# Optimization experiments

Hardware: AMD Instinct MI355X
Metric: run time of the kernel (lower is better)

Reference implementation:

```python
import jax, jax.numpy as jnp
import numpy as np

N_HEAD = 16

def setup_inputs() -> dict:
    key = jax.random.key(0)
    k1, k2, k3 = jax.random.split(key, 3)
    B, T, C = 4, 2048, 1024
    x = jax.random.normal(k1, (B, T, C), dtype=jnp.float32)
    w_attn = jax.random.normal(k2, (C, 3 * C), dtype=jnp.float32) * 0.02
    w_o = jax.random.normal(k3, (C, C), dtype=jnp.float32) * 0.02
    return {"x": x, "w_attn": w_attn, "w_o": w_o}

def reference(x, w_attn, w_o):
    B, T, C = x.shape
    H = N_HEAD
    hs = C // H
    qkv = x @ w_attn  # [B,T,3C]
    q, k, v = jnp.split(qkv, 3, axis=-1)
    # [B,H,T,hs]
    q = q.reshape(B, T, H, hs).transpose(0, 2, 1, 3)
    k = k.reshape(B, T, H, hs).transpose(0, 2, 1, 3)
    v = v.reshape(B, T, H, hs).transpose(0, 2, 1, 3)
    att = jnp.einsum('bhqd,bhkd->bhqk', q, k) * (1.0 / np.sqrt(hs).astype(np.float32))
    causal = jnp.tril(jnp.ones((T, T), dtype=bool))
    att = jnp.where(causal[None, None], att, jnp.float32(-jnp.inf))
    att = jax.nn.softmax(att, axis=-1)
    y = jnp.einsum('bhqk,bhkd->bhqd', att, v)
    y = y.transpose(0, 2, 1, 3).reshape(B, T, C)
    return y @ w_o
```

## Files before the change

### kernel.cpp

```cpp
#include <hip/hip_runtime.h>

typedef unsigned short u16;
typedef unsigned int u32;
typedef __attribute__((ext_vector_type(8))) __bf16 bf16x8;
typedef __attribute__((ext_vector_type(4))) float f32x4;
typedef __attribute__((ext_vector_type(8))) unsigned short u16x8;
typedef __attribute__((ext_vector_type(4))) unsigned int u32x4;

typedef const __attribute__((address_space(1))) u32 gu32;
typedef __attribute__((address_space(3))) u32 lu32;

__device__ __forceinline__ u16 f2b(float f) {
  u32 u = __builtin_bit_cast(u32, f);
  u32 r = u + 0x7fffu + ((u >> 16) & 1u);
  return (u16)(r >> 16);
}

__device__ __forceinline__ u32 pk2(float lo, float hi) {
  u32 d;
  asm("v_cvt_pk_bf16_f32 %0, %1, %2" : "=v"(d) : "v"(lo), "v"(hi));
  return d;
}

__device__ __forceinline__ bf16x8 pack8(f32x4 a, f32x4 b) {
  u32x4 u;
  u[0] = pk2(a[0], a[1]);
  u[1] = pk2(a[2], a[3]);
  u[2] = pk2(b[0], b[1]);
  u[3] = pk2(b[2], b[3]);
  return __builtin_bit_cast(bf16x8, u);
}

__device__ __forceinline__ bf16x8 ld8(const u16* p) {
  return __builtin_bit_cast(bf16x8, *(const u16x8*)p);
}

__device__ __forceinline__ void gll16(const void* g, void* l) {
  __builtin_amdgcn_global_load_lds((gu32*)g, (lu32*)l, 16, 0, 0);
}

__device__ __forceinline__ f32x4 mfma16(bf16x8 a, bf16x8 b, f32x4 c) {
  return __builtin_amdgcn_mfma_f32_16x16x32_bf16(a, b, c, 0, 0, 0);
}

__global__ void k_cvt(const float* __restrict__ in, u16* __restrict__ out, int n4) {
  int i = blockIdx.x * blockDim.x + threadIdx.x;
  int stride = gridDim.x * blockDim.x;
  for (int idx = i; idx < n4; idx += stride) {
    float4 v = ((const float4*)in)[idx];
    u32 lo = (u32)f2b(v.x) | ((u32)f2b(v.y) << 16);
    u32 hi = (u32)f2b(v.z) | ((u32)f2b(v.w) << 16);
    ((uint2*)out)[idx] = make_uint2(lo, hi);
  }
}

__global__ void k_tr(const float* __restrict__ in, u16* __restrict__ out, int R, int C) {
  __shared__ u16 tile[32][33];
  int bx = blockIdx.x * 32;
  int by = blockIdx.y * 32;
  int tx = threadIdx.x, ty = threadIdx.y;
#pragma unroll
  for (int i = 0; i < 32; i += 8)
    tile[ty + i][tx] = f2b(in[(size_t)(by + ty + i) * C + bx + tx]);
  __syncthreads();
#pragma unroll
  for (int i = 0; i < 32; i += 8)
    out[(size_t)(bx + ty + i) * R + by + tx] = tile[tx][ty + i];
}

template <int EPI>
__global__ __launch_bounds__(256) void k_gemm(const u16* __restrict__ A,
                                              const u16* __restrict__ B,
                                              void* __restrict__ Cp) {
  const int K = 1024;
  const int NT = 32;
  __shared__ __align__(16) u16 As[2][128 * 32];
  __shared__ __align__(16) u16 Bs[2][128 * 32];
  int tid = threadIdx.x;
  int lane = tid & 63, wid = tid >> 6;
  int wr = wid >> 1, wc = wid & 1;
  int m0 = blockIdx.y * 128, n0 = blockIdx.x * 128;
  int r = lane & 15, qq = lane >> 4;

  int schunk = (lane & 3) ^ ((lane >> 3) & 3);
  const u16* Ag0 = A + (size_t)(m0 + wid * 32 + (lane >> 2)) * K + schunk * 8;
  const u16* Bg0 = B + (size_t)(n0 + wid * 32 + (lane >> 2)) * K + schunk * 8;
  int sl0 = (wid * 32) * 32;
  int sl1 = (wid * 32 + 16) * 32;
  int rsw = (qq ^ ((r >> 1) & 3)) * 8;

#define GSTAGE(buf, k0)                          \
  do {                                           \
    gll16(Ag0 + (k0), &As[buf][sl0]);            \
    gll16(Ag0 + 16 * K + (k0), &As[buf][sl1]);   \
    gll16(Bg0 + (k0), &Bs[buf][sl0]);            \
    gll16(Bg0 + 16 * K + (k0), &Bs[buf][sl1]);   \
  } while (0)

  f32x4 acc[4][4] = {};

  GSTAGE(0, 0);
  GSTAGE(1, 32);

  for (int kt = 0; kt < NT; ++kt) {
    int cur = kt & 1;
    if (kt + 1 < NT)
      asm volatile("s_waitcnt vmcnt(4)" ::: "memory");
    else
      asm volatile("s_waitcnt vmcnt(0)" ::: "memory");
    __builtin_amdgcn_s_barrier();

    bf16x8 af[4], bfr[4];
#pragma unroll
    for (int m = 0; m < 4; ++m)
      af[m] = ld8(&As[cur][(wr * 64 + m * 16 + r) * 32 + rsw]);
#pragma unroll
    for (int n = 0; n < 4; ++n)
      bfr[n] = ld8(&Bs[cur][(wc * 64 + n * 16 + r) * 32 + rsw]);
    asm volatile("s_waitcnt lgkmcnt(0)" ::: "memory");
    __builtin_amdgcn_sched_barrier(0);
    __builtin_amdgcn_s_barrier();

    if (kt + 2 < NT) GSTAGE(cur, (kt + 2) * 32);

#pragma unroll
    for (int m = 0; m < 4; ++m)
#pragma unroll
      for (int n = 0; n < 4; ++n) acc[m][n] = mfma16(af[m], bfr[n], acc[m][n]);
  }
#undef GSTAGE

  if constexpr (EPI == 0) {
    u16* qkv = (u16*)Cp;
#pragma unroll
    for (int m = 0; m < 4; ++m) {
      int gr = m0 + wr * 64 + m * 16 + qq * 4;
      int b = gr >> 11, t0 = gr & 2047;
#pragma unroll
      for (int n = 0; n < 4; ++n) {
        int gc = n0 + wc * 64 + n * 16 + r;
        int which = gc >> 10, rem = gc & 1023;
        int hh = rem >> 6, d = rem & 63;
        if (which == 2) {
          u16* dst = qkv + (size_t)2 * 8388608u +
                     ((size_t)((b * 16 + hh) * 64 + d)) * 2048 + t0;
          u32 p0 = pk2(acc[m][n][0], acc[m][n][1]);
          u32 p1 = pk2(acc[m][n][2], acc[m][n][3]);
          *(uint2*)dst = make_uint2(p0, p1);
        } else {
          float sc = (which == 0) ? 0.18033688011112042f : 1.0f;
          u16* dst = qkv + (size_t)which * 8388608u +
                     ((size_t)((b * 16 + hh) * 2048 + t0)) * 64 + d;
#pragma unroll
          for (int i = 0; i < 4; ++i) dst[(size_t)i * 64] = f2b(acc[m][n][i] * sc);
        }
      }
    }
  } else {
    float* out = (float*)Cp;
#pragma unroll
    for (int m = 0; m < 4; ++m) {
      int gr = m0 + wr * 64 + m * 16 + qq * 4;
#pragma unroll
      for (int n = 0; n < 4; ++n) {
        int gc = n0 + wc * 64 + n * 16 + r;
#pragma unroll
        for (int i = 0; i < 4; ++i) out[(size_t)(gr + i) * 1024 + gc] = acc[m][n][i];
      }
    }
  }
}

__global__ __launch_bounds__(256) void k_attn(const u16* __restrict__ Qm,
                                              const u16* __restrict__ Km,
                                              const u16* __restrict__ VTm,
                                              u16* __restrict__ Y) {
  int bi = blockIdx.x;
  int p = bi >> 6;
  int bh = bi & 63;
  int b = bh >> 4, h = bh & 15;
  int tid = threadIdx.x, lane = tid & 63, w = tid >> 6;
  int r = lane & 15, qq = lane >> 4;
  const size_t base = (size_t)bh * (2048 * 64);

  __shared__ __align__(16) u16 Kt[2][64 * 64];
  __shared__ __align__(16) u16 Vt[2][64 * 64];

  int srow = lane >> 3;
  int kch0 = (lane & 7) ^ (srow & 3);
  int kch1 = (lane & 7) ^ ((srow & 3) | 4);
  int vch = (lane & 7) ^ srow;
  const u16* Kg = Km + base;
  const u16* Vg = VTm + base;

  int ar = 8 * (r >> 2) + (r & 3);
  int fkl = (r & 3) | (((r >> 2) & 1) << 2);
  int ks0 = ((qq ^ fkl)) * 8, ks1 = ((qq ^ fkl) ^ 4) * 8;
  int fvl = r & 7;
  int vs0 = ((qq ^ fvl)) * 8, vs1 = ((qq ^ fvl) ^ 4) * 8;

#define STAGE(buf, j0n)                                                                 \
  do {                                                                                  \
    gll16(Kg + (size_t)((j0n) + w * 16 + srow) * 64 + kch0 * 8,                         \
          &Kt[buf][(w * 16) * 64]);                                                     \
    gll16(Kg + (size_t)((j0n) + w * 16 + 8 + srow) * 64 + kch1 * 8,                     \
          &Kt[buf][(w * 16 + 8) * 64]);                                                 \
    gll16(Vg + (size_t)(w * 16 + srow) * 2048 + (j0n) + vch * 8,                        \
          &Vt[buf][(w * 16) * 64]);                                                     \
    gll16(Vg + (size_t)(w * 16 + 8 + srow) * 2048 + (j0n) + vch * 8,                    \
          &Vt[buf][(w * 16 + 8) * 64]);                                                 \
  } while (0)

  for (int ph = 0; ph < 2; ++ph) {
    int qb = (ph == 0) ? (15 - p) : p;
    int qb0 = qb * 128;
    int q0w = qb0 + w * 32;

    bf16x8 qf[2][2];
#pragma unroll
    for (int m = 0; m < 2; ++m)
#pragma unroll
      for (int kc = 0; kc < 2; ++kc)
        qf[m][kc] = ld8(Qm + base + (size_t)(q0w + m * 16 + r) * 64 + kc * 32 + qq * 8);

    f32x4 acc[2][4] = {};
    float m_run[2] = {-1e30f, -1e30f};
    float l_run[2] = {0.f, 0.f};
    int ntwg = (qb0 >> 6) + 2;

    STAGE(0, 0);
    __syncthreads();

    for (int it = 0; it < ntwg; ++it) {
      int j0 = it << 6;
      int cur = it & 1;
      bool active = (j0 <= q0w + 31);
      f32x4 s[4][2];
      bf16x8 vfr[4][2];

      if (active) {
        __builtin_amdgcn_s_setprio(1);
#pragma unroll
        for (int nt = 0; nt < 4; ++nt) {
          int knt = 32 * (nt >> 1) + 4 * (nt & 1);
          const u16* kb_ = &Kt[cur][(knt + ar) * 64];
          bf16x8 k0 = ld8(kb_ + ks0);
          bf16x8 k1 = ld8(kb_ + ks1);
#pragma unroll
          for (int m = 0; m < 2; ++m) {
            f32x4 z = {};
            s[nt][m] = mfma16(k1, qf[m][1], mfma16(k0, qf[m][0], z));
          }
        }
#pragma unroll
        for (int n = 0; n < 4; ++n) {
          const u16* vb_ = &Vt[cur][(n * 16 + r) * 64];
          vfr[n][0] = ld8(vb_ + vs0);
          vfr[n][1] = ld8(vb_ + vs1);
        }
        __builtin_amdgcn_s_setprio(0);
      }

      if (it + 1 < ntwg) STAGE(cur ^ 1, j0 + 64);

      if (active) {
        bool nm = (j0 + 63 > q0w);
        if (nm) {
#pragma unroll
          for (int nt = 0; nt < 4; ++nt) {
            int kb = j0 + 32 * (nt >> 1) + 4 * (nt & 1) + 8 * qq;
#pragma unroll
            for (int m = 0; m < 2; ++m) {
              int qg = q0w + m * 16 + r;
#pragma unroll
              for (int i = 0; i < 4; ++i)
                s[nt][m][i] = (kb + i <= qg) ? s[nt][m][i] : -1e30f;
            }
          }
        }

        float tm[2];
#pragma unroll
        for (int m = 0; m < 2; ++m) {
          float t0 = fmaxf(fmaxf(s[0][m][0], s[0][m][1]), fmaxf(s[0][m][2], s[0][m][3]));
          float t1 = fmaxf(fmaxf(s[1][m][0], s[1][m][1]), fmaxf(s[1][m][2], s[1][m][3]));
          float t2 = fmaxf(fmaxf(s[2][m][0], s[2][m][1]), fmaxf(s[2][m][2], s[2][m][3]));
          float t3 = fmaxf(fmaxf(s[3][m][0], s[3][m][1]), fmaxf(s[3][m][2], s[3][m][3]));
          float t = fmaxf(fmaxf(t0, t1), fmaxf(t2, t3));
          t = fmaxf(t, __shfl_xor(t, 16));
          t = fmaxf(t, __shfl_xor(t, 32));
          tm[m] = t;
        }

        int grow = (tm[0] > m_run[0]) | (tm[1] > m_run[1]);
        if (__any(grow)) {
#pragma unroll
          for (int m = 0; m < 2; ++m) {
            float mn = fmaxf(m_run[m], tm[m]);
            float corr = __builtin_amdgcn_exp2f(m_run[m] - mn);
            m_run[m] = mn;
            l_run[m] *= corr;
#pragma unroll
            for (int i = 0; i < 4; ++i) {
              float c = __shfl(corr, qq * 4 + i);
#pragma unroll
              for (int n = 0; n < 4; ++n) acc[m][n][i] *= c;
            }
          }
        }

#pragma unroll
        for (int m = 0; m < 2; ++m) {
          float ls = 0.f;
#pragma unroll
          for (int nt = 0; nt < 4; ++nt)
#pragma unroll
            for (int i = 0; i < 4; ++i) {
              float e = __builtin_amdgcn_exp2f(s[nt][m][i] - m_run[m]);
              s[nt][m][i] = e;
              ls += e;
            }
          l_run[m] += ls;
        }

        __builtin_amdgcn_s_setprio(1);
#pragma unroll
        for (int m = 0; m < 2; ++m) {
          bf16x8 pa0 = pack8(s[0][m], s[1][m]);
          bf16x8 pa1 = pack8(s[2][m], s[3][m]);
#pragma unroll
          for (int n = 0; n < 4; ++n) acc[m][n] = mfma16(pa0, vfr[n][0], acc[m][n]);
#pragma unroll
          for (int n = 0; n < 4; ++n) acc[m][n] = mfma16(pa1, vfr[n][1], acc[m][n]);
        }
        __builtin_amdgcn_s_setprio(0);
      }

      __syncthreads();
    }

    float li[2][4];
#pragma unroll
    for (int m = 0; m < 2; ++m) {
      float l = l_run[m];
      l += __shfl_xor(l, 16);
      l += __shfl_xor(l, 32);
      float inv = 1.0f / l;
#pragma unroll
      for (int i = 0; i < 4; ++i) li[m][i] = __shfl(inv, qq * 4 + i);
    }
#pragma unroll
    for (int m = 0; m < 2; ++m)
#pragma unroll
      for (int n = 0; n < 4; ++n)
#pragma unroll
        for (int i = 0; i < 4; ++i)
          Y[((size_t)(b * 2048 + q0w + m * 16 + qq * 4 + i)) * 1024 + h * 64 + n * 16 +
            r] = f2b(acc[m][n][i] * li[m][i]);
  }
#undef STAGE
}

extern "C" void kernel_launch(void* const* d_in, const int* in_sizes, int n_in,
                              void* d_out, int out_size, void* d_ws, size_t ws_size,
                              hipStream_t stream) {
  const float* x = (const float*)d_in[0];
  const float* w_attn = (const float*)d_in[1];
  const float* w_o = (const float*)d_in[2];
  float* out = (float*)d_out;

  char* ws = (char*)d_ws;
  u16* xb = (u16*)(ws + 0);
  u16* watT = (u16*)(ws + 16777216);
  u16* woT = (u16*)(ws + 23068672);
  u16* qb = (u16*)(ws + 25165824);
  u16* kb = (u16*)(ws + 41943040);
  u16* vb = (u16*)(ws + 58720256);
  u16* yb = (u16*)(ws + 75497472);

  k_cvt<<<2048, 256, 0, stream>>>(x, xb, 8192 * 1024 / 4);
  k_tr<<<dim3(3072 / 32, 1024 / 32), dim3(32, 8), 0, stream>>>(w_attn, watT, 1024, 3072);
  k_tr<<<dim3(1024 / 32, 1024 / 32), dim3(32, 8), 0, stream>>>(w_o, woT, 1024, 1024);
  k_gemm<0><<<dim3(24, 64), 256, 0, stream>>>(xb, watT, (void*)qb);
  k_attn<<<dim3(512), 256, 0, stream>>>(qb, kb, vb, yb);
  k_gemm<1><<<dim3(8, 64), 256, 0, stream>>>(yb, woT, (void*)out);
}
```

Before: 185.3 us.

## Split attention KV loop across two wave groups and merge partial softmax

```diff
diff --git a/kernel.cpp b/kernel.cpp
--- a/kernel.cpp
+++ b/kernel.cpp
@@ -171,7 +171,7 @@
   }
 }
 
-__global__ __launch_bounds__(256) void k_attn(const u16* __restrict__ Qm,
+__global__ __launch_bounds__(512) void k_attn(const u16* __restrict__ Qm,
                                               const u16* __restrict__ Km,
                                               const u16* __restrict__ VTm,
                                               u16* __restrict__ Y) {
@@ -180,11 +180,12 @@
   int bh = bi & 63;
   int b = bh >> 4, h = bh & 15;
   int tid = threadIdx.x, lane = tid & 63, w = tid >> 6;
+  int g = w >> 2, wl = w & 3;
   int r = lane & 15, qq = lane >> 4;
   const size_t base = (size_t)bh * (2048 * 64);
 
-  __shared__ __align__(16) u16 Kt[2][64 * 64];
-  __shared__ __align__(16) u16 Vt[2][64 * 64];
+  __shared__ __align__(16) u16 Kt[2][2][64 * 64];
+  __shared__ __align__(16) u16 Vt[2][2][64 * 64];
 
   int srow = lane >> 3;
   int kch0 = (lane & 7) ^ (srow & 3);
@@ -199,22 +200,22 @@
   int fvl = r & 7;
   int vs0 = ((qq ^ fvl)) * 8, vs1 = ((qq ^ fvl) ^ 4) * 8;
 
-#define STAGE(buf, j0n)                                                                 \
+#define STAGE(par, j0n)                                                                 \
   do {                                                                                  \
-    gll16(Kg + (size_t)((j0n) + w * 16 + srow) * 64 + kch0 * 8,                         \
-          &Kt[buf][(w * 16) * 64]);                                                     \
-    gll16(Kg + (size_t)((j0n) + w * 16 + 8 + srow) * 64 + kch1 * 8,                     \
-          &Kt[buf][(w * 16 + 8) * 64]);                                                 \
-    gll16(Vg + (size_t)(w * 16 + srow) * 2048 + (j0n) + vch * 8,                        \
-          &Vt[buf][(w * 16) * 64]);                                                     \
-    gll16(Vg + (size_t)(w * 16 + 8 + srow) * 2048 + (j0n) + vch * 8,                    \
-          &Vt[buf][(w * 16 + 8) * 64]);                                                 \
+    gll16(Kg + (size_t)((j0n) + wl * 16 + srow) * 64 + kch0 * 8,                        \
+          &Kt[par][g][(wl * 16) * 64]);                                                 \
+    gll16(Kg + (size_t)((j0n) + wl * 16 + 8 + srow) * 64 + kch1 * 8,                    \
+          &Kt[par][g][(wl * 16 + 8) * 64]);                                             \
+    gll16(Vg + (size_t)(wl * 16 + srow) * 2048 + (j0n) + vch * 8,                       \
+          &Vt[par][g][(wl * 16) * 64]);                                                 \
+    gll16(Vg + (size_t)(wl * 16 + 8 + srow) * 2048 + (j0n) + vch * 8,                   \
+          &Vt[par][g][(wl * 16 + 8) * 64]);                                             \
   } while (0)
 
   for (int ph = 0; ph < 2; ++ph) {
     int qb = (ph == 0) ? (15 - p) : p;
     int qb0 = qb * 128;
-    int q0w = qb0 + w * 32;
+    int q0w = qb0 + wl * 32;
 
     bf16x8 qf[2][2];
 #pragma unroll
@@ -226,14 +227,14 @@
     f32x4 acc[2][4] = {};
     float m_run[2] = {-1e30f, -1e30f};
     float l_run[2] = {0.f, 0.f};
-    int ntwg = (qb0 >> 6) + 2;
-
-    STAGE(0, 0);
+    int npairs = qb + 1;
+
+    STAGE(0, g << 6);
     __syncthreads();
 
-    for (int it = 0; it < ntwg; ++it) {
-      int j0 = it << 6;
-      int cur = it & 1;
+    for (int t2 = 0; t2 < npairs; ++t2) {
+      int j0 = (t2 << 7) + (g << 6);
+      int cur = t2 & 1;
       bool active = (j0 <= q0w + 31);
       f32x4 s[4][2];
       bf16x8 vfr[4][2];
@@ -243,7 +244,7 @@
 #pragma unroll
         for (int nt = 0; nt < 4; ++nt) {
           int knt = 32 * (nt >> 1) + 4 * (nt & 1);
-          const u16* kb_ = &Kt[cur][(knt + ar) * 64];
+          const u16* kb_ = &Kt[cur][g][(knt + ar) * 64];
           bf16x8 k0 = ld8(kb_ + ks0);
           bf16x8 k1 = ld8(kb_ + ks1);
 #pragma unroll
@@ -254,14 +255,14 @@
         }
 #pragma unroll
         for (int n = 0; n < 4; ++n) {
-          const u16* vb_ = &Vt[cur][(n * 16 + r) * 64];
+          const u16* vb_ = &Vt[cur][g][(n * 16 + r) * 64];
           vfr[n][0] = ld8(vb_ + vs0);
           vfr[n][1] = ld8(vb_ + vs1);
         }
         __builtin_amdgcn_s_setprio(0);
       }
 
-      if (it + 1 < ntwg) STAGE(cur ^ 1, j0 + 64);
+      if (t2 + 1 < npairs) STAGE((t2 + 1) & 1, ((t2 + 1) << 7) + (g << 6));
 
       if (active) {
         bool nm = (j0 + 63 > q0w);
@@ -284,9 +285,9 @@
         for (int m = 0; m < 2; ++m) {
           float t0 = fmaxf(fmaxf(s[0][m][0], s[0][m][1]), fmaxf(s[0][m][2], s[0][m][3]));
           float t1 = fmaxf(fmaxf(s[1][m][0], s[1][m][1]), fmaxf(s[1][m][2], s[1][m][3]));
-          float t2 = fmaxf(fmaxf(s[2][m][0], s[2][m][1]), fmaxf(s[2][m][2], s[2][m][3]));
+          float t2f = fmaxf(fmaxf(s[2][m][0], s[2][m][1]), fmaxf(s[2][m][2], s[2][m][3]));
           float t3 = fmaxf(fmaxf(s[3][m][0], s[3][m][1]), fmaxf(s[3][m][2], s[3][m][3]));
-          float t = fmaxf(fmaxf(t0, t1), fmaxf(t2, t3));
+          float t = fmaxf(fmaxf(t0, t1), fmaxf(t2f, t3));
           t = fmaxf(t, __shfl_xor(t, 16));
           t = fmaxf(t, __shfl_xor(t, 32));
           tm[m] = t;
@@ -339,24 +340,63 @@
       __syncthreads();
     }
 
-    float li[2][4];
+    float lfin[2];
 #pragma unroll
     for (int m = 0; m < 2; ++m) {
       float l = l_run[m];
       l += __shfl_xor(l, 16);
       l += __shfl_xor(l, 32);
-      float inv = 1.0f / l;
-#pragma unroll
-      for (int i = 0; i < 4; ++i) li[m][i] = __shfl(inv, qq * 4 + i);
-    }
-#pragma unroll
-    for (int m = 0; m < 2; ++m)
+      lfin[m] = l;
+    }
+
+    float* mgK = (float*)&Kt[0][0][0];
+    float* mgV = (float*)&Vt[0][0][0];
+    int offA = wl * 1104 + lane * 17;
+    int offM = 4608 + wl * 320 + lane * 5;
+    if (g == 1) {
 #pragma unroll
       for (int n = 0; n < 4; ++n)
 #pragma unroll
-        for (int i = 0; i < 4; ++i)
-          Y[((size_t)(b * 2048 + q0w + m * 16 + qq * 4 + i)) * 1024 + h * 64 + n * 16 +
-            r] = f2b(acc[m][n][i] * li[m][i]);
+        for (int i = 0; i < 4; ++i) {
+          mgK[offA + n * 4 + i] = acc[0][n][i];
+          mgV[offA + n * 4 + i] = acc[1][n][i];
+        }
+      mgK[offM + 0] = m_run[0];
+      mgK[offM + 1] = m_run[1];
+      mgK[offM + 2] = lfin[0];
+      mgK[offM + 3] = lfin[1];
+    }
+    __syncthreads();
+
+    if (g == 0) {
+      float fA[2], fB[2];
+#pragma unroll
+      for (int m = 0; m < 2; ++m) {
+        float mB = mgK[offM + m];
+        float lB = mgK[offM + 2 + m];
+        float mM = fmaxf(m_run[m], mB);
+        float cA = __builtin_amdgcn_exp2f(m_run[m] - mM);
+        float cB = __builtin_amdgcn_exp2f(mB - mM);
+        float inv = 1.0f / (lfin[m] * cA + lB * cB);
+        fA[m] = cA * inv;
+        fB[m] = cB * inv;
+      }
+#pragma unroll
+      for (int m = 0; m < 2; ++m)
+#pragma unroll
+        for (int i = 0; i < 4; ++i) {
+          float a = __shfl(fA[m], qq * 4 + i);
+          float bq = __shfl(fB[m], qq * 4 + i);
+          float* mg = (m == 0) ? mgK : mgV;
+#pragma unroll
+          for (int n = 0; n < 4; ++n) {
+            float o = acc[m][n][i] * a + mg[offA + n * 4 + i] * bq;
+            Y[((size_t)(b * 2048 + q0w + m * 16 + qq * 4 + i)) * 1024 + h * 64 +
+              n * 16 + r] = f2b(o);
+          }
+        }
+    }
+    __syncthreads();
   }
 #undef STAGE
 }
@@ -382,6 +422,6 @@
   k_tr<<<dim3(3072 / 32, 1024 / 32), dim3(32, 8), 0, stream>>>(w_attn, watT, 1024, 3072);
   k_tr<<<dim3(1024 / 32, 1024 / 32), dim3(32, 8), 0, stream>>>(w_o, woT, 1024, 1024);
   k_gemm<0><<<dim3(24, 64), 256, 0, stream>>>(xb, watT, (void*)qb);
-  k_attn<<<dim3(512), 256, 0, stream>>>(qb, kb, vb, yb);
+  k_attn<<<dim3(512), 512, 0, stream>>>(qb, kb, vb, yb);
   k_gemm<1><<<dim3(8, 64), 256, 0, stream>>>(yb, woT, (void*)out);
 }
```

After: 184.1 us. Within noise of the previous version (-0.7%).
